# Optimization experiments

Hardware: AMD Instinct MI355X
Metric: run time of the kernel (lower is better)

The kernel has to match this reference:

```python
import jax, jax.numpy as jnp
import numpy as np

DIM = 512
HEADS = 16
HEAD_DIM = DIM // HEADS
SCALE = HEAD_DIM ** -0.5


def setup_inputs() -> dict:
    key = jax.random.key(0)
    k = jax.random.split(key, 6)
    B_, N = 2048, 49
    nW = 64
    x = jax.random.normal(k[0], (B_, N, DIM), dtype=jnp.float32)
    mask = jax.random.normal(k[1], (nW, N, N), dtype=jnp.float32)
    W_qkv = jax.random.normal(k[2], (3 * DIM, DIM), dtype=jnp.float32) * 0.02
    b_qkv = jnp.zeros((3 * DIM,), dtype=jnp.float32)
    W_proj = jax.random.normal(k[3], (DIM, DIM), dtype=jnp.float32) * 0.02
    b_proj = jnp.zeros((DIM,), dtype=jnp.float32)
    return {"x": x, "mask": mask, "W_qkv": W_qkv, "b_qkv": b_qkv,
            "W_proj": W_proj, "b_proj": b_proj}


def reference(x, mask, W_qkv, b_qkv, W_proj, b_proj):
    B_, N, C = x.shape
    H, d = HEADS, HEAD_DIM
    nW = mask.shape[0]
    # qkv projection: [B_, N, 3, H, d] -> q,k,v each [B_, H, N, d]
    qkv = (x @ W_qkv.T + b_qkv).reshape(B_, N, 3, H, d)
    qkv = jnp.transpose(qkv, (2, 0, 3, 1, 4))
    q, k, v = qkv[0], qkv[1], qkv[2]
    attn = jnp.einsum('bhnd,bhmd->bhnm', q * SCALE, k)  # [B_, H, N, N]
    # add per-window additive mask, broadcast over B_//nW groups and heads
    attn = attn.reshape(B_ // nW, nW, H, N, N) + mask[None, :, None, :, :]
    attn = attn.reshape(B_, H, N, N)
    attn = jax.nn.softmax(attn, axis=-1)
    out = jnp.einsum('bhnm,bhmd->bhnd', attn, v)  # [B_, H, N, d]
    out = jnp.transpose(out, (0, 2, 1, 3)).reshape(B_, N, C)
    return out @ W_proj.T + b_proj
```

## Files before the change

### kernel.cpp

```cpp
#include <hip/hip_runtime.h>


typedef unsigned short ushort_t;
typedef __bf16 bf16x8 __attribute__((ext_vector_type(8)));
typedef float f32x4 __attribute__((ext_vector_type(4)));
typedef unsigned short us8 __attribute__((ext_vector_type(8)));

#define SCALE_F 0.17677669529663687f
constexpr size_t QKV_REG = 2048ULL * 16 * 49 * 32;

__device__ __forceinline__ ushort_t f2bf(float f) {
  unsigned u = __builtin_bit_cast(unsigned, f);
  u += 0x7FFFu + ((u >> 16) & 1u);
  return (ushort_t)(u >> 16);
}

__device__ __forceinline__ void gload_lds16(const void* g, void* l) {
  __builtin_amdgcn_global_load_lds(
      (const __attribute__((address_space(1))) void*)g,
      (__attribute__((address_space(3))) void*)l, 16, 0, 0);
}

__global__ __launch_bounds__(256) void k_cvt(const float* __restrict__ in,
                                             ushort_t* __restrict__ out, int n4) {
  int i = blockIdx.x * blockDim.x + threadIdx.x;
  if (i >= n4) return;
  float4 v = reinterpret_cast<const float4*>(in)[i];
  ushort4 o = make_ushort4(f2bf(v.x), f2bf(v.y), f2bf(v.z), f2bf(v.w));
  reinterpret_cast<ushort4*>(out)[i] = o;
}

template <int EPI>
__global__ __launch_bounds__(256) void k_gemm(const ushort_t* __restrict__ A,
                                              const ushort_t* __restrict__ W,
                                              const float* __restrict__ bias,
                                              ushort_t* __restrict__ out_qkv,
                                              float* __restrict__ out_f,
                                              int nt_o) {
  __shared__ __align__(16) ushort_t As[128][64];
  __shared__ __align__(16) ushort_t Ws[128][64];

  const int tid  = threadIdx.x;
  const int lane = tid & 63;
  const int wv   = tid >> 6;
  const int wr   = wv >> 1, wc = wv & 1;

  const int cpx = gridDim.x >> 3;
  const int lid = (blockIdx.x & 7) * cpx + (blockIdx.x >> 3);
  const int bm  = lid / nt_o;
  const int bo  = lid - bm * nt_o;
  const size_t m0 = (size_t)bm * 128;
  const int o0    = bo * 128;

  f32x4 acc[4][4];
#pragma unroll
  for (int i = 0; i < 4; i++)
#pragma unroll
    for (int j = 0; j < 4; j++) acc[i][j] = f32x4{0.f, 0.f, 0.f, 0.f};

  const int srow   = wv * 32 + (lane >> 3);
  const int schunk = (((lane & 7) ^ (lane >> 3)) * 8);

  for (int kt = 0; kt < 8; ++kt) {
    const int k0 = kt * 64;
#pragma unroll
    for (int i = 0; i < 4; i++) {
      const ushort_t* g = A + (m0 + srow + i * 8) * 512 + k0 + schunk;
      gload_lds16(g, &As[wv * 32 + i * 8][0]);
    }
#pragma unroll
    for (int i = 0; i < 4; i++) {
      const ushort_t* g = W + (size_t)(o0 + srow + i * 8) * 512 + k0 + schunk;
      gload_lds16(g, &Ws[wv * 32 + i * 8][0]);
    }
    __syncthreads();
    const int fr = lane & 15;
#pragma unroll
    for (int kk = 0; kk < 2; ++kk) {
      const int ch = kk * 4 + (lane >> 4);
      const int cb = ((ch ^ (lane & 7)) << 3);
      uint4 ar[4], br[4];
#pragma unroll
      for (int mi = 0; mi < 4; mi++)
        ar[mi] = *reinterpret_cast<const uint4*>(&As[wr * 64 + mi * 16 + fr][cb]);
#pragma unroll
      for (int ni = 0; ni < 4; ni++)
        br[ni] = *reinterpret_cast<const uint4*>(&Ws[wc * 64 + ni * 16 + fr][cb]);
#pragma unroll
      for (int mi = 0; mi < 4; mi++)
#pragma unroll
        for (int ni = 0; ni < 4; ni++)
          acc[mi][ni] = __builtin_amdgcn_mfma_f32_16x16x32_bf16(
              __builtin_bit_cast(bf16x8, ar[mi]),
              __builtin_bit_cast(bf16x8, br[ni]), acc[mi][ni], 0, 0, 0);
    }
    __syncthreads();
  }

  const int colbase = lane & 15;
  const int rowgrp  = (lane >> 4) * 4;

  if constexpr (EPI == 1) {
#pragma unroll
    for (int ni = 0; ni < 4; ni++) {
      const int o = o0 + wc * 64 + ni * 16 + colbase;
      const float bv = bias[o];
#pragma unroll
      for (int mi = 0; mi < 4; mi++) {
        const size_t mrow = m0 + wr * 64 + mi * 16 + rowgrp;
#pragma unroll
        for (int r = 0; r < 4; r++)
          out_f[(mrow + r) * 512 + o] = acc[mi][ni][r] + bv;
      }
    }
  } else {
#pragma unroll
    for (int mi = 0; mi < 4; mi++) {
#pragma unroll
      for (int r = 0; r < 4; r++) {
        const int t = (int)m0 + wr * 64 + mi * 16 + rowgrp + r;
        const int b = t / 49;
        const int n = t - b * 49;
#pragma unroll
        for (int ni = 0; ni < 4; ni++) {
          const int o = o0 + wc * 64 + ni * 16 + colbase;
          const int which = o >> 9;
          const int h = (o >> 5) & 15;
          const int dd = o & 31;
          const size_t dst = (size_t)which * QKV_REG +
                             (((size_t)b * 16 + h) * 49 + n) * 32 + dd;
          out_qkv[dst] = f2bf(acc[mi][ni][r] + bias[o]);
        }
      }
    }
  }
}

__global__ __launch_bounds__(256) void k_attn(const ushort_t* __restrict__ qkv,
                                              const float* __restrict__ mask,
                                              ushort_t* __restrict__ aout) {
  __shared__ __align__(16) ushort_t Vt[32][64];
  __shared__ __align__(16) ushort_t Ps[4][16][64];

  const int tid  = threadIdx.x;
  const int lane = tid & 63;
  const int mt   = tid >> 6;
  const int bh   = blockIdx.x;
  const int b    = bh >> 4, h = bh & 15;
  const int w    = b & 63;
  const size_t base = (size_t)bh * (49 * 32);
  const ushort_t* qb = qkv + base;
  const ushort_t* kb = qkv + QKV_REG + base;
  const ushort_t* vb = qkv + 2 * QKV_REG + base;

  reinterpret_cast<uint4*>(&Vt[0][0])[tid] = make_uint4(0, 0, 0, 0);
  __syncthreads();
  if (tid < 196) {
    const int n = tid >> 2, d0 = (tid & 3) * 8;
    uint4 raw = *reinterpret_cast<const uint4*>(vb + n * 32 + d0);
    us8 e = __builtin_bit_cast(us8, raw);
#pragma unroll
    for (int j = 0; j < 8; j++) {
      Vt[d0 + j][(((n >> 3) ^ j) << 3) | (n & 7)] = e[j];
    }
  }
  __syncthreads();

  const int arow = lane & 15;
  const int kc   = (lane >> 4) * 8;

  uint4 qraw = *reinterpret_cast<const uint4*>(qb + (mt * 16 + arow) * 32 + kc);
  bf16x8 qa = __builtin_bit_cast(bf16x8, qraw);
  f32x4 s[4];
#pragma unroll
  for (int ni = 0; ni < 4; ni++) {
    uint4 kraw = *reinterpret_cast<const uint4*>(kb + (ni * 16 + arow) * 32 + kc);
    f32x4 z = {0.f, 0.f, 0.f, 0.f};
    s[ni] = __builtin_amdgcn_mfma_f32_16x16x32_bf16(
        qa, __builtin_bit_cast(bf16x8, kraw), z, 0, 0, 0);
  }

  const int rg = (lane >> 4) * 4;
  float rsum[4];
#pragma unroll
  for (int r = 0; r < 4; r++) {
    const int qr = mt * 16 + rg + r;
    float sv[4];
    float mx = -1e30f;
#pragma unroll
    for (int ni = 0; ni < 4; ni++) {
      const int col = ni * 16 + arow;
      float v;
      if (qr < 49 && col < 49)
        v = s[ni][r] * SCALE_F + mask[(size_t)w * 2401 + qr * 49 + col];
      else
        v = -1e30f;
      sv[ni] = v;
      mx = fmaxf(mx, v);
    }
#pragma unroll
    for (int off = 1; off < 16; off <<= 1) mx = fmaxf(mx, __shfl_xor(mx, off));
    float sum = 0.f;
    const int prow = rg + r;
#pragma unroll
    for (int ni = 0; ni < 4; ni++) {
      float p = __expf(sv[ni] - mx);
      sum += p;
      const int pcol = ni * 16 + arow;
      Ps[mt][prow][(((pcol >> 3) ^ (prow & 7)) << 3) | (pcol & 7)] = f2bf(p);
    }
#pragma unroll
    for (int off = 1; off < 16; off <<= 1) sum += __shfl_xor(sum, off);
    rsum[r] = sum;
  }

  __syncthreads();

  f32x4 o0 = {0.f, 0.f, 0.f, 0.f}, o1 = {0.f, 0.f, 0.f, 0.f};
#pragma unroll
  for (int kk = 0; kk < 2; kk++) {
    const int ch = kk * 4 + (lane >> 4);
    const int cb = ((ch ^ (lane & 7)) << 3);
    uint4 praw = *reinterpret_cast<const uint4*>(&Ps[mt][arow][cb]);
    bf16x8 pa = __builtin_bit_cast(bf16x8, praw);
    uint4 v0 = *reinterpret_cast<const uint4*>(&Vt[arow][cb]);
    uint4 v1 = *reinterpret_cast<const uint4*>(&Vt[16 + arow][cb]);
    o0 = __builtin_amdgcn_mfma_f32_16x16x32_bf16(pa, __builtin_bit_cast(bf16x8, v0), o0, 0, 0, 0);
    o1 = __builtin_amdgcn_mfma_f32_16x16x32_bf16(pa, __builtin_bit_cast(bf16x8, v1), o1, 0, 0, 0);
  }

#pragma unroll
  for (int r = 0; r < 4; r++) {
    const int qr = mt * 16 + rg + r;
    if (qr < 49) {
      const float inv = 1.f / rsum[r];
      aout[((size_t)b * 49 + qr) * 512 + h * 32 + arow]      = f2bf(o0[r] * inv);
      aout[((size_t)b * 49 + qr) * 512 + h * 32 + 16 + arow] = f2bf(o1[r] * inv);
    }
  }
}

extern "C" void kernel_launch(void* const* d_in, const int* in_sizes, int n_in,
                              void* d_out, int out_size, void* d_ws, size_t ws_size,
                              hipStream_t stream) {
  const float* x      = (const float*)d_in[0];
  const float* mask   = (const float*)d_in[1];
  const float* W_qkv  = (const float*)d_in[2];
  const float* b_qkv  = (const float*)d_in[3];
  const float* W_proj = (const float*)d_in[4];
  const float* b_proj = (const float*)d_in[5];
  float* out = (float*)d_out;

  ushort_t* ws     = (ushort_t*)d_ws;
  ushort_t* xb     = ws;
  ushort_t* qkvb   = ws + 51380224UL;
  ushort_t* aoutb  = ws + 205520896UL;
  ushort_t* wqkvb  = ws + 256901120UL;
  ushort_t* wprojb = ws + 257687552UL;

  const int n4x = 51380224 / 4, n4q = 786432 / 4, n4p = 262144 / 4;
  k_cvt<<<(n4x + 255) / 256, 256, 0, stream>>>(x, xb, n4x);
  k_cvt<<<(n4q + 255) / 256, 256, 0, stream>>>(W_qkv, wqkvb, n4q);
  k_cvt<<<(n4p + 255) / 256, 256, 0, stream>>>(W_proj, wprojb, n4p);

  k_gemm<0><<<784 * 12, 256, 0, stream>>>(xb, wqkvb, b_qkv, qkvb, nullptr, 12);

  k_attn<<<2048 * 16, 256, 0, stream>>>(qkvb, mask, aoutb);

  k_gemm<1><<<784 * 4, 256, 0, stream>>>(aoutb, wprojb, b_proj, nullptr, out, 4);
}
```

Baseline: 592.9 us.

## Assign one attention head per wave with four heads per block

New measurement: 574.7 us. 1.03x faster.

```diff
diff --git a/kernel.cpp b/kernel.cpp
--- a/kernel.cpp
+++ b/kernel.cpp
@@ -64,15 +64,13 @@
   for (int kt = 0; kt < 8; ++kt) {
     const int k0 = kt * 64;
 #pragma unroll
-    for (int i = 0; i < 4; i++) {
-      const ushort_t* g = A + (m0 + srow + i * 8) * 512 + k0 + schunk;
-      gload_lds16(g, &As[wv * 32 + i * 8][0]);
-    }
-#pragma unroll
-    for (int i = 0; i < 4; i++) {
-      const ushort_t* g = W + (size_t)(o0 + srow + i * 8) * 512 + k0 + schunk;
-      gload_lds16(g, &Ws[wv * 32 + i * 8][0]);
-    }
+    for (int i = 0; i < 4; i++)
+      gload_lds16(A + (m0 + srow + i * 8) * 512 + k0 + schunk,
+                  &As[wv * 32 + i * 8][0]);
+#pragma unroll
+    for (int i = 0; i < 4; i++)
+      gload_lds16(W + (size_t)(o0 + srow + i * 8) * 512 + k0 + schunk,
+                  &Ws[wv * 32 + i * 8][0]);
     __syncthreads();
     const int fr = lane & 15;
 #pragma unroll
@@ -136,106 +134,140 @@
   }
 }
 
-__global__ __launch_bounds__(256) void k_attn(const ushort_t* __restrict__ qkv,
-                                              const float* __restrict__ mask,
-                                              ushort_t* __restrict__ aout) {
-  __shared__ __align__(16) ushort_t Vt[32][64];
-  __shared__ __align__(16) ushort_t Ps[4][16][64];
+__global__ __launch_bounds__(256) void k_attn4(const ushort_t* __restrict__ qkv,
+                                               const float* __restrict__ mask,
+                                               ushort_t* __restrict__ aout) {
+  __shared__ __align__(16) ushort_t Vt[4][32][64];
+  __shared__ __align__(16) ushort_t Ps[4][64][64];
 
   const int tid  = threadIdx.x;
   const int lane = tid & 63;
-  const int mt   = tid >> 6;
-  const int bh   = blockIdx.x;
-  const int b    = bh >> 4, h = bh & 15;
+  const int wv   = tid >> 6;
+  const int blk  = blockIdx.x;
+  const int b    = blk >> 2;
+  const int h    = (blk & 3) * 4 + wv;
   const int w    = b & 63;
-  const size_t base = (size_t)bh * (49 * 32);
+  const size_t base = (((size_t)b * 16 + h)) * (49 * 32);
   const ushort_t* qb = qkv + base;
   const ushort_t* kb = qkv + QKV_REG + base;
   const ushort_t* vb = qkv + 2 * QKV_REG + base;
 
-  reinterpret_cast<uint4*>(&Vt[0][0])[tid] = make_uint4(0, 0, 0, 0);
+  {
+    uint4* vz = reinterpret_cast<uint4*>(&Vt[wv][0][0]);
+#pragma unroll
+    for (int i = 0; i < 4; i++) vz[i * 64 + lane] = make_uint4(0, 0, 0, 0);
+  }
   __syncthreads();
-  if (tid < 196) {
-    const int n = tid >> 2, d0 = (tid & 3) * 8;
-    uint4 raw = *reinterpret_cast<const uint4*>(vb + n * 32 + d0);
-    us8 e = __builtin_bit_cast(us8, raw);
-#pragma unroll
-    for (int j = 0; j < 8; j++) {
-      Vt[d0 + j][(((n >> 3) ^ j) << 3) | (n & 7)] = e[j];
-    }
-  }
-  __syncthreads();
+#pragma unroll
+  for (int i = 0; i < 4; i++) {
+    const int e = lane + (i << 6);
+    if (e < 196) {
+      const int n = e >> 2, d0 = (e & 3) * 8;
+      uint4 raw = *reinterpret_cast<const uint4*>(vb + n * 32 + d0);
+      us8 ev = __builtin_bit_cast(us8, raw);
+#pragma unroll
+      for (int j = 0; j < 8; j++)
+        Vt[wv][d0 + j][(((n >> 3) ^ j) << 3) | (n & 7)] = ev[j];
+    }
+  }
 
   const int arow = lane & 15;
   const int kc   = (lane >> 4) * 8;
-
-  uint4 qraw = *reinterpret_cast<const uint4*>(qb + (mt * 16 + arow) * 32 + kc);
-  bf16x8 qa = __builtin_bit_cast(bf16x8, qraw);
-  f32x4 s[4];
-#pragma unroll
-  for (int ni = 0; ni < 4; ni++) {
-    uint4 kraw = *reinterpret_cast<const uint4*>(kb + (ni * 16 + arow) * 32 + kc);
-    f32x4 z = {0.f, 0.f, 0.f, 0.f};
-    s[ni] = __builtin_amdgcn_mfma_f32_16x16x32_bf16(
-        qa, __builtin_bit_cast(bf16x8, kraw), z, 0, 0, 0);
-  }
-
-  const int rg = (lane >> 4) * 4;
-  float rsum[4];
-#pragma unroll
-  for (int r = 0; r < 4; r++) {
-    const int qr = mt * 16 + rg + r;
-    float sv[4];
-    float mx = -1e30f;
-#pragma unroll
-    for (int ni = 0; ni < 4; ni++) {
-      const int col = ni * 16 + arow;
-      float v;
-      if (qr < 49 && col < 49)
-        v = s[ni][r] * SCALE_F + mask[(size_t)w * 2401 + qr * 49 + col];
-      else
-        v = -1e30f;
-      sv[ni] = v;
-      mx = fmaxf(mx, v);
-    }
-#pragma unroll
-    for (int off = 1; off < 16; off <<= 1) mx = fmaxf(mx, __shfl_xor(mx, off));
-    float sum = 0.f;
-    const int prow = rg + r;
-#pragma unroll
-    for (int ni = 0; ni < 4; ni++) {
-      float p = __expf(sv[ni] - mx);
-      sum += p;
-      const int pcol = ni * 16 + arow;
-      Ps[mt][prow][(((pcol >> 3) ^ (prow & 7)) << 3) | (pcol & 7)] = f2bf(p);
-    }
-#pragma unroll
-    for (int off = 1; off < 16; off <<= 1) sum += __shfl_xor(sum, off);
-    rsum[r] = sum;
+  const int rg   = (lane >> 4) * 4;
+
+  uint4 kf[4];
+#pragma unroll
+  for (int ni = 0; ni < 4; ni++)
+    kf[ni] = *reinterpret_cast<const uint4*>(kb + (ni * 16 + arow) * 32 + kc);
+
+  float rsum[4][4];
+
+#pragma unroll
+  for (int hm = 0; hm < 2; hm++) {
+    f32x4 s2[2][4];
+#pragma unroll
+    for (int j = 0; j < 2; j++) {
+      const int mt = hm * 2 + j;
+      uint4 qraw = *reinterpret_cast<const uint4*>(qb + (mt * 16 + arow) * 32 + kc);
+      bf16x8 qa = __builtin_bit_cast(bf16x8, qraw);
+#pragma unroll
+      for (int ni = 0; ni < 4; ni++) {
+        f32x4 z = {0.f, 0.f, 0.f, 0.f};
+        s2[j][ni] = __builtin_amdgcn_mfma_f32_16x16x32_bf16(
+            qa, __builtin_bit_cast(bf16x8, kf[ni]), z, 0, 0, 0);
+      }
+    }
+#pragma unroll
+    for (int j = 0; j < 2; j++) {
+      const int mt = hm * 2 + j;
+#pragma unroll
+      for (int r = 0; r < 4; r++) {
+        const int qr = mt * 16 + rg + r;
+        float sv[4];
+        float mx = -1e30f;
+#pragma unroll
+        for (int ni = 0; ni < 4; ni++) {
+          const int col = ni * 16 + arow;
+          float v;
+          if (qr < 49 && col < 49)
+            v = s2[j][ni][r] * SCALE_F + mask[(size_t)w * 2401 + qr * 49 + col];
+          else
+            v = -1e30f;
+          sv[ni] = v;
+          mx = fmaxf(mx, v);
+        }
+#pragma unroll
+        for (int off = 1; off < 16; off <<= 1) mx = fmaxf(mx, __shfl_xor(mx, off));
+        float sum = 0.f;
+        const int prow = rg + r;
+#pragma unroll
+        for (int ni = 0; ni < 4; ni++) {
+          float p = __expf(sv[ni] - mx);
+          sum += p;
+          const int pcol = ni * 16 + arow;
+          Ps[wv][mt * 16 + prow]
+            [(((pcol >> 3) ^ (prow & 7)) << 3) | (pcol & 7)] = f2bf(p);
+        }
+#pragma unroll
+        for (int off = 1; off < 16; off <<= 1) sum += __shfl_xor(sum, off);
+        rsum[mt][r] = sum;
+      }
+    }
   }
 
   __syncthreads();
 
-  f32x4 o0 = {0.f, 0.f, 0.f, 0.f}, o1 = {0.f, 0.f, 0.f, 0.f};
+  uint4 vf0[2], vf1[2];
 #pragma unroll
   for (int kk = 0; kk < 2; kk++) {
     const int ch = kk * 4 + (lane >> 4);
     const int cb = ((ch ^ (lane & 7)) << 3);
-    uint4 praw = *reinterpret_cast<const uint4*>(&Ps[mt][arow][cb]);
-    bf16x8 pa = __builtin_bit_cast(bf16x8, praw);
-    uint4 v0 = *reinterpret_cast<const uint4*>(&Vt[arow][cb]);
-    uint4 v1 = *reinterpret_cast<const uint4*>(&Vt[16 + arow][cb]);
-    o0 = __builtin_amdgcn_mfma_f32_16x16x32_bf16(pa, __builtin_bit_cast(bf16x8, v0), o0, 0, 0, 0);
-    o1 = __builtin_amdgcn_mfma_f32_16x16x32_bf16(pa, __builtin_bit_cast(bf16x8, v1), o1, 0, 0, 0);
-  }
-
-#pragma unroll
-  for (int r = 0; r < 4; r++) {
-    const int qr = mt * 16 + rg + r;
-    if (qr < 49) {
-      const float inv = 1.f / rsum[r];
-      aout[((size_t)b * 49 + qr) * 512 + h * 32 + arow]      = f2bf(o0[r] * inv);
-      aout[((size_t)b * 49 + qr) * 512 + h * 32 + 16 + arow] = f2bf(o1[r] * inv);
+    vf0[kk] = *reinterpret_cast<const uint4*>(&Vt[wv][arow][cb]);
+    vf1[kk] = *reinterpret_cast<const uint4*>(&Vt[wv][16 + arow][cb]);
+  }
+
+#pragma unroll
+  for (int mt = 0; mt < 4; mt++) {
+    f32x4 o0 = {0.f, 0.f, 0.f, 0.f}, o1 = {0.f, 0.f, 0.f, 0.f};
+#pragma unroll
+    for (int kk = 0; kk < 2; kk++) {
+      const int ch = kk * 4 + (lane >> 4);
+      const int cb = ((ch ^ (lane & 7)) << 3);
+      uint4 praw = *reinterpret_cast<const uint4*>(&Ps[wv][mt * 16 + arow][cb]);
+      bf16x8 pa = __builtin_bit_cast(bf16x8, praw);
+      o0 = __builtin_amdgcn_mfma_f32_16x16x32_bf16(
+          pa, __builtin_bit_cast(bf16x8, vf0[kk]), o0, 0, 0, 0);
+      o1 = __builtin_amdgcn_mfma_f32_16x16x32_bf16(
+          pa, __builtin_bit_cast(bf16x8, vf1[kk]), o1, 0, 0, 0);
+    }
+#pragma unroll
+    for (int r = 0; r < 4; r++) {
+      const int qr = mt * 16 + rg + r;
+      if (qr < 49) {
+        const float inv = 1.f / rsum[mt][r];
+        aout[((size_t)b * 49 + qr) * 512 + h * 32 + arow]      = f2bf(o0[r] * inv);
+        aout[((size_t)b * 49 + qr) * 512 + h * 32 + 16 + arow] = f2bf(o1[r] * inv);
+      }
     }
   }
 }
@@ -265,7 +297,7 @@
 
   k_gemm<0><<<784 * 12, 256, 0, stream>>>(xb, wqkvb, b_qkv, qkvb, nullptr, 12);
 
-  k_attn<<<2048 * 16, 256, 0, stream>>>(qkvb, mask, aoutb);
+  k_attn4<<<2048 * 4, 256, 0, stream>>>(qkvb, mask, aoutb);
 
   k_gemm<1><<<784 * 4, 256, 0, stream>>>(aoutb, wprojb, b_proj, nullptr, out, 4);
 }
```
